# Performance work log

Hardware: AMD Instinct MI355X
Metric: run time of the kernel (lower is better)

Reference implementation:

```python
import jax, jax.numpy as jnp
import numpy as np

N = 50000          # num nodes
E = 800000         # num edges (before self loops)
DIM_IN = 128
HID = 32           # per-head hidden of conv1
HEADS = 8          # heads of conv1
DIM_OUT = 16       # output classes (conv2, 1 head, concat=False)
NEG_SLOPE = 0.2    # GATConv default leaky_relu slope


def gat_conv(x, W, a_src, a_dst, bias, src, dst, heads, out_ch, concat):
    """PyG GATConv (self-loops already appended to src/dst).
    x: [N, F_in], W: [F_in, heads*out_ch], a_src/a_dst: [heads, out_ch], bias matches output.
    """
    n = x.shape[0]
    h = (x @ W).reshape(n, heads, out_ch)                    # [N, H, C]
    al_src = jnp.einsum('nhc,hc->nh', h, a_src)              # [N, H]
    al_dst = jnp.einsum('nhc,hc->nh', h, a_dst)              # [N, H]
    e = jax.nn.leaky_relu(al_src[src] + al_dst[dst], NEG_SLOPE)   # [E', H]
    # segment softmax over edges grouped by target node (dst)
    emax = jax.ops.segment_max(e, dst, num_segments=n)       # [N, H]
    ee = jnp.exp(e - emax[dst])                              # [E', H]
    denom = jax.ops.segment_sum(ee, dst, num_segments=n)     # [N, H]
    alpha = ee / (denom[dst] + 1e-16)                        # [E', H]
    msg = h[src] * alpha[:, :, None]                         # [E', H, C]
    out = jax.ops.segment_sum(msg, dst, num_segments=n)      # [N, H, C]
    out = out.reshape(n, heads * out_ch) if concat else out.mean(axis=1)
    return out + bias


def setup_inputs() -> dict:
    key = jax.random.key(0)
    ks = jax.random.split(key, 12)
    x = jax.random.normal(ks[0], (N, DIM_IN), dtype=jnp.float32)
    edge_index = jax.random.randint(ks[1], (2, E), 0, N, dtype=jnp.int64)
    s = 0.1
    W1 = jax.random.normal(ks[2], (DIM_IN, HEADS * HID), dtype=jnp.float32) * s
    a1_src = jax.random.normal(ks[3], (HEADS, HID), dtype=jnp.float32) * s
    a1_dst = jax.random.normal(ks[4], (HEADS, HID), dtype=jnp.float32) * s
    b1 = jnp.zeros((HEADS * HID,), dtype=jnp.float32)
    W2 = jax.random.normal(ks[5], (HEADS * HID, DIM_OUT), dtype=jnp.float32) * s
    a2_src = jax.random.normal(ks[6], (1, DIM_OUT), dtype=jnp.float32) * s
    a2_dst = jax.random.normal(ks[7], (1, DIM_OUT), dtype=jnp.float32) * s
    b2 = jnp.zeros((DIM_OUT,), dtype=jnp.float32)
    return {"x": x, "edge_index": edge_index, "W1": W1, "a1_src": a1_src,
            "a1_dst": a1_dst, "b1": b1, "W2": W2, "a2_src": a2_src,
            "a2_dst": a2_dst, "b2": b2}


def reference(x, edge_index, W1, a1_src, a1_dst, b1, W2, a2_src, a2_dst, b2):
    # add self loops (GATConv default add_self_loops=True)
    loops = jnp.arange(N, dtype=edge_index.dtype)
    src = jnp.concatenate([edge_index[0], loops])
    dst = jnp.concatenate([edge_index[1], loops])
    # dropout layers are identity in eval mode
    h = gat_conv(x, W1, a1_src, a1_dst, b1, src, dst, HEADS, HID, concat=True)
    h = jax.nn.elu(h)
    out = gat_conv(h, W2, a2_src, a2_dst, b2, src, dst, 1, DIM_OUT, concat=False)
    return jax.nn.log_softmax(out, axis=1)
```

## Files before the change

kernel.cpp:

```cpp
#include <hip/hip_runtime.h>
#include <hip/hip_bf16.h>

#define NN 50000
#define EE 800000
#define EP (EE + NN)
#define DIN 128
#define HID 32
#define HEADS 8
#define C1 (HEADS * HID)
#define DOUT 16
#define NW1 3125
#define SH 8
#define NB 196
#define CAP 8192
#define EPT 8
#define BBLK (256 * EPT)
#define GB ((NW1 * 64 + 255) / 256)
#define BB ((EP + BBLK - 1) / BBLK)

typedef __attribute__((ext_vector_type(8))) short short8;
typedef __attribute__((ext_vector_type(4))) float float4v;
typedef __attribute__((ext_vector_type(2))) float float2v;

__device__ inline unsigned short f2bf(float f) {
    __hip_bfloat16 b = __float2bfloat16(f);
    return *reinterpret_cast<unsigned short*>(&b);
}
__device__ inline float bflo(unsigned u) {
    union { unsigned int i; float f; } x;
    x.i = u << 16;
    return x.f;
}
__device__ inline float bfhi(unsigned u) {
    union { unsigned int i; float f; } x;
    x.i = u & 0xffff0000u;
    return x.f;
}
__device__ inline float bf2f(unsigned short u) {
    union { unsigned int i; float f; } x;
    x.i = ((unsigned int)u) << 16;
    return x.f;
}

__global__ void k_prepfw(const float* __restrict__ W1, const float* __restrict__ a1s,
                         const float* __restrict__ a1d, const float* __restrict__ W2,
                         unsigned short* __restrict__ w1frag,
                         unsigned short* __restrict__ w2frag,
                         int* __restrict__ cntb) {
    int i = blockIdx.x * 256 + threadIdx.x;
    if (blockIdx.x == 0 && threadIdx.x < NB) cntb[threadIdx.x] = 0;
    if (i < 17 * 2048) {
        int j = i & 7, lane = (i >> 3) & 63, s = (i >> 9) & 3, c = i >> 11;
        int q = lane >> 4, m = lane & 15;
        int k = s * 32 + q * 8 + j;
        float val;
        if (c < 16) {
            val = W1[k * C1 + c * 16 + m];
        } else {
            int h = m & 7;
            const float* av = (m < 8) ? a1s : a1d;
            float acc = 0.f;
            #pragma unroll
            for (int j2 = 0; j2 < 32; j2++)
                acc += W1[k * C1 + h * 32 + j2] * av[h * 32 + j2];
            val = acc;
        }
        w1frag[i] = f2bf(val);
    } else if (i < 17 * 2048 + 8 * 512) {
        int j2 = i - 17 * 2048;
        int jj = j2 & 7, lane = (j2 >> 3) & 63, s = j2 >> 9;
        int q = lane >> 4, m = lane & 15;
        w2frag[j2] = f2bf(W2[(s * 32 + q * 8 + jj) * DOUT + m]);
    }
}

__global__ __launch_bounds__(256) void k_g1bkt(const float* __restrict__ x,
                                               const unsigned short* __restrict__ w1frag,
                                               unsigned char* __restrict__ h1f8,
                                               float* __restrict__ al1sd,
                                               unsigned short* __restrict__ al1s8,
                                               const int* __restrict__ ei,
                                               int* __restrict__ cntb,
                                               unsigned* __restrict__ ebuf) {
    __shared__ int hist[4][NB];
    __shared__ int base[4][NB];
    int bid = blockIdx.x;
    if (bid < GB) {
        int wid = (bid * 256 + threadIdx.x) >> 6;
        int lane = threadIdx.x & 63;
        if (wid >= NW1) return;
        int nb = wid * 16;
        int m = lane & 15, quad = lane >> 4;
        const float* xrow = x + (nb + m) * DIN;

        float4 xf[8];
        #pragma unroll
        for (int s = 0; s < 4; s++) {
            xf[2 * s]     = *(const float4*)(xrow + s * 32 + quad * 8);
            xf[2 * s + 1] = *(const float4*)(xrow + s * 32 + quad * 8 + 4);
        }
        short8 bfr[4];
        #pragma unroll
        for (int s = 0; s < 4; s++) {
            unsigned short* bp = (unsigned short*)&bfr[s];
            float4 f0 = xf[2 * s], f1 = xf[2 * s + 1];
            bp[0] = f2bf(f0.x); bp[1] = f2bf(f0.y); bp[2] = f2bf(f0.z); bp[3] = f2bf(f0.w);
            bp[4] = f2bf(f1.x); bp[5] = f2bf(f1.y); bp[6] = f2bf(f1.z); bp[7] = f2bf(f1.w);
        }

        float4v acc[17];
        #pragma unroll
        for (int c = 0; c < 17; c++) acc[c] = (float4v){0.f, 0.f, 0.f, 0.f};

        #pragma unroll
        for (int s = 0; s < 4; s++) {
            const unsigned short* fp = w1frag + (s * 64 + lane) * 8;
            #pragma unroll
            for (int c = 0; c < 17; c++) {
                short8 afrag = *(const short8*)(fp + c * 2048);
                acc[c] = __builtin_amdgcn_mfma_f32_16x16x32_bf16(afrag, bfr[s], acc[c], 0, 0, 0);
            }
        }

        int node = nb + m;
        #pragma unroll
        for (int c = 0; c < 16; c++) {
            unsigned pk = 0;
            pk = __builtin_amdgcn_cvt_pk_fp8_f32(acc[c][0], acc[c][1], pk, false);
            pk = __builtin_amdgcn_cvt_pk_fp8_f32(acc[c][2], acc[c][3], pk, true);
            *(unsigned*)(h1f8 + node * C1 + c * 16 + quad * 4) = pk;
        }
        *(float4*)(al1sd + node * 16 + quad * 4) =
            make_float4(acc[16][0], acc[16][1], acc[16][2], acc[16][3]);
        if (quad < 2) {
            uint2 pk;
            pk.x = (unsigned)f2bf(acc[16][0]) | ((unsigned)f2bf(acc[16][1]) << 16);
            pk.y = (unsigned)f2bf(acc[16][2]) | ((unsigned)f2bf(acc[16][3]) << 16);
            *(uint2*)(al1s8 + node * 8 + quad * 4) = pk;
        }
    } else {
        int t = threadIdx.x;
        int wave = t >> 6;
        for (int i = t; i < 4 * NB; i += 256) ((int*)hist)[i] = 0;
        __syncthreads();
        int e0 = (bid - GB) * BBLK;
        int s[EPT], d[EPT], r[EPT];
        #pragma unroll
        for (int j = 0; j < EPT; j++) {
            int e = e0 + j * 256 + t;
            int ss = 0, dd = -1;
            if (e < EE) { ss = ei[e]; dd = ei[EE + e]; }
            else if (e < EP) { ss = e - EE; dd = ss; }
            s[j] = ss; d[j] = dd;
            if (dd >= 0) r[j] = atomicAdd(&hist[wave][dd >> SH], 1);
        }
        __syncthreads();
        if (t < NB) {
            int h0 = hist[0][t], h1 = hist[1][t], h2 = hist[2][t], h3 = hist[3][t];
            int tot = h0 + h1 + h2 + h3;
            int bb = tot ? atomicAdd(&cntb[t], tot) : 0;
            base[0][t] = bb;
            base[1][t] = bb + h0;
            base[2][t] = bb + h0 + h1;
            base[3][t] = bb + h0 + h1 + h2;
        }
        __syncthreads();
        #pragma unroll
        for (int j = 0; j < EPT; j++) {
            if (d[j] >= 0) {
                int b = d[j] >> SH;
                ebuf[b * CAP + base[wave][b] + r[j]] =
                    ((unsigned)s[j] << SH) | (unsigned)(d[j] & 255);
            }
        }
    }
}

__global__ __launch_bounds__(1024) void k_csr(const int* __restrict__ cntb,
                                              const unsigned* __restrict__ ebuf,
                                              int* __restrict__ row_ptr,
                                              int* __restrict__ esrc) {
    __shared__ int sdeg[256];
    __shared__ int wtot[4];
    __shared__ int bpart[4];
    int b = blockIdx.x;
    int t = threadIdx.x;
    int lane = t & 63, wave = t >> 6;
    int nodes0 = b << SH;
    if (t < 256) sdeg[t] = 0;
    if (t < 256) {
        int v = (t < b) ? cntb[t] : 0;
        #pragma unroll
        for (int off = 1; off < 64; off <<= 1) v += __shfl_xor(v, off, 64);
        if (lane == 0) bpart[wave] = v;
    }
    __syncthreads();
    int baseS = bpart[0] + bpart[1] + bpart[2] + bpart[3];
    int cnt = cntb[b];
    const unsigned* eb = ebuf + b * CAP;
    for (int i = t; i < cnt; i += 1024)
        atomicAdd(&sdeg[eb[i] & 255], 1);
    __syncthreads();
    int v = (t < 256) ? sdeg[t] : 0;
    int inc = v;
    #pragma unroll
    for (int off = 1; off < 64; off <<= 1) {
        int u = __shfl_up(inc, off, 64);
        if (lane >= off) inc += u;
    }
    if (t < 256 && lane == 63) wtot[wave] = inc;
    __syncthreads();
    if (wave == 0 && lane < 4) {
        int w = wtot[lane];
        int iw = w;
        #pragma unroll
        for (int off = 1; off < 4; off <<= 1) {
            int u = __shfl_up(iw, off, 64);
            if (lane >= off) iw += u;
        }
        wtot[lane] = iw - w;
    }
    __syncthreads();
    int excl = inc - v + ((t < 256) ? wtot[wave] : 0);
    __syncthreads();
    if (t < 256) {
        sdeg[t] = excl;
        int node = nodes0 + t;
        if (node < NN) row_ptr[node] = baseS + excl;
    }
    __syncthreads();
    for (int i = t; i < cnt; i += 1024) {
        unsigned e = eb[i];
        int pos = atomicAdd(&sdeg[e & 255], 1);
        esrc[baseS + pos] = (int)(e >> SH);
    }
    if (b == 0 && t == 0) row_ptr[NN] = EP;
}

__global__ __launch_bounds__(256) void k_agg1(const int* __restrict__ row_ptr,
                                              const int* __restrict__ esrc,
                                              const unsigned short* __restrict__ al1s8,
                                              const float* __restrict__ al1sd,
                                              const unsigned char* __restrict__ h1f8,
                                              const float* __restrict__ b1,
                                              unsigned short* __restrict__ helu_b) {
    int L = threadIdx.x & 63;
    int d = __builtin_amdgcn_readfirstlane((int)((blockIdx.x * 256 + threadIdx.x) >> 6));
    int start = row_ptr[d], end = row_ptr[d + 1];
    const int Lofs = L * 4;
    const int hprod = L & 7;
    const int egrp  = L >> 3;
    float ald_p = al1sd[d * 16 + 8 + hprod];
    float denom = 0.f;
    float4 acc = make_float4(0.f, 0.f, 0.f, 0.f);

    for (int base = start; base < end; base += 32) {
        int cnt = min(32, end - base);
        int sval = d;
        if (L < cnt) sval = esrc[base + L];
        float asv0, asv1, asv2, asv3;
        {
            int sp0 = __shfl(sval, 0 * 8 + egrp, 64);
            int sp1 = __shfl(sval, 1 * 8 + egrp, 64);
            int sp2 = __shfl(sval, 2 * 8 + egrp, 64);
            int sp3 = __shfl(sval, 3 * 8 + egrp, 64);
            asv0 = bf2f(al1s8[sp0 * 8 + hprod]);
            asv1 = bf2f(al1s8[sp1 * 8 + hprod]);
            asv2 = bf2f(al1s8[sp2 * 8 + hprod]);
            asv3 = bf2f(al1s8[sp3 * 8 + hprod]);
        }
        #define AGG1_GROUP(K, ASV)                                              \
        if (cnt > (K) * 8) {                                                    \
            float e = (ASV) + ald_p;                                            \
            e = e > 0.f ? e : 0.2f * e;                                         \
            float w = ((K) * 8 + egrp < cnt) ? __expf(e) : 0.f;                 \
            unsigned v[8];                                                      \
            float xw[8];                                                        \
            _Pragma("unroll")                                                   \
            for (int j = 0; j < 8; j++) {                                       \
                int sj = __builtin_amdgcn_readlane(sval, (K) * 8 + j);          \
                v[j] = *(const unsigned*)(h1f8 + sj * C1 + Lofs);               \
                xw[j] = __shfl(w, j * 8 + egrp, 64);                            \
            }                                                                   \
            _Pragma("unroll")                                                   \
            for (int j = 0; j < 8; j++) {                                       \
                float2v a = __builtin_amdgcn_cvt_pk_f32_fp8(v[j], false);       \
                float2v b = __builtin_amdgcn_cvt_pk_f32_fp8(v[j], true);        \
                float xj = xw[j];                                               \
                denom += xj;                                                    \
                acc.x += xj * a.x; acc.y += xj * a.y;                           \
                acc.z += xj * b.x; acc.w += xj * b.y;                           \
            }                                                                   \
        }
        AGG1_GROUP(0, asv0)
        AGG1_GROUP(1, asv1)
        AGG1_GROUP(2, asv2)
        AGG1_GROUP(3, asv3)
        #undef AGG1_GROUP
    }
    float inv = 1.0f / (denom + 1e-16f);
    float4 bv = *(const float4*)(b1 + Lofs);
    float o0 = acc.x * inv + bv.x;
    float o1 = acc.y * inv + bv.y;
    float o2 = acc.z * inv + bv.z;
    float o3 = acc.w * inv + bv.w;
    o0 = o0 > 0.f ? o0 : __expf(o0) - 1.0f;
    o1 = o1 > 0.f ? o1 : __expf(o1) - 1.0f;
    o2 = o2 > 0.f ? o2 : __expf(o2) - 1.0f;
    o3 = o3 > 0.f ? o3 : __expf(o3) - 1.0f;
    uint2 pk;
    pk.x = (unsigned)f2bf(o0) | ((unsigned)f2bf(o1) << 16);
    pk.y = (unsigned)f2bf(o2) | ((unsigned)f2bf(o3) << 16);
    *(uint2*)(helu_b + d * C1 + Lofs) = pk;
}

__global__ __launch_bounds__(256) void k_gemm2(const unsigned short* __restrict__ helu_b,
                                               const unsigned short* __restrict__ w2frag,
                                               const float* __restrict__ a2s,
                                               const float* __restrict__ a2d,
                                               unsigned short* __restrict__ h2b,
                                               float* __restrict__ al2s,
                                               float* __restrict__ al2d) {
    int wid = (blockIdx.x * 256 + threadIdx.x) >> 6;
    int lane = threadIdx.x & 63;
    int nb = wid * 16;
    if (nb >= NN) return;
    int m = lane & 15, quad = lane >> 4;

    const unsigned short* wp2 = w2frag + lane * 8;
    float4v acc = {0.f, 0.f, 0.f, 0.f};
    const unsigned short* arow = helu_b + (nb + m) * C1 + quad * 8;
    #pragma unroll
    for (int s = 0; s < 8; s++) {
        short8 afrag = *(const short8*)(arow + s * 32);
        short8 bfrag = *(const short8*)(wp2 + s * 512);
        acc = __builtin_amdgcn_mfma_f32_16x16x32_bf16(afrag, bfrag, acc, 0, 0, 0);
    }

    float as_c = a2s[m], ad_c = a2d[m];
    #pragma unroll
    for (int r = 0; r < 4; r++) {
        int node = nb + quad * 4 + r;
        float val = acc[r];
        h2b[node * DOUT + m] = f2bf(val);
        float ps = val * as_c;
        float pd = val * ad_c;
        ps += __shfl_xor(ps, 1, 64); ps += __shfl_xor(ps, 2, 64);
        ps += __shfl_xor(ps, 4, 64); ps += __shfl_xor(ps, 8, 64);
        pd += __shfl_xor(pd, 1, 64); pd += __shfl_xor(pd, 2, 64);
        pd += __shfl_xor(pd, 4, 64); pd += __shfl_xor(pd, 8, 64);
        if (m == 0) {
            al2s[node] = ps;
            al2d[node] = pd;
        }
    }
}

__global__ __launch_bounds__(256) void k_agg2(const int* __restrict__ row_ptr,
                                              const int* __restrict__ esrc,
                                              const unsigned short* __restrict__ h2b,
                                              const float* __restrict__ al2s,
                                              const float* __restrict__ al2d,
                                              const float* __restrict__ b2,
                                              float* __restrict__ out) {
    int L = threadIdx.x & 63;
    int n = __builtin_amdgcn_readfirstlane((int)((blockIdx.x * 256 + threadIdx.x) >> 6));
    int p = L & 7, g = L >> 3;
    int start = row_ptr[n], end = row_ptr[n + 1];
    float ald = al2d[n];
    float acc0 = 0.f, acc1 = 0.f, denom = 0.f;

    for (int base = start; base < end; base += 64) {
        int cnt = min(64, end - base);
        int sval = n; float w = 0.f;
        if (L < cnt) {
            sval = esrc[base + L];
            float e = al2s[sval] + ald;
            e = e > 0.f ? e : 0.2f * e;
            w = __expf(e);
        }
        unsigned v0, v1, v2, v3, v4, v5, v6, v7;
        float w0, w1, w2, w3, w4, w5, w6, w7;
        #define AGG2_LOAD(K, V, W)                                             \
        if (cnt > (K) * 8) {                                                   \
            int ss = __shfl(sval, (K) * 8 + g, 64);                            \
            W = __shfl(w, (K) * 8 + g, 64);                                    \
            V = *(const unsigned*)(h2b + ss * DOUT + p * 2);                   \
        }
        AGG2_LOAD(0, v0, w0) AGG2_LOAD(1, v1, w1)
        AGG2_LOAD(2, v2, w2) AGG2_LOAD(3, v3, w3)
        AGG2_LOAD(4, v4, w4) AGG2_LOAD(5, v5, w5)
        AGG2_LOAD(6, v6, w6) AGG2_LOAD(7, v7, w7)
        #undef AGG2_LOAD
        #define AGG2_ACC(K, V, W)                                              \
        if (cnt > (K) * 8) {                                                   \
            acc0 += W * bflo(V); acc1 += W * bfhi(V); denom += W;              \
        }
        AGG2_ACC(0, v0, w0) AGG2_ACC(1, v1, w1)
        AGG2_ACC(2, v2, w2) AGG2_ACC(3, v3, w3)
        AGG2_ACC(4, v4, w4) AGG2_ACC(5, v5, w5)
        AGG2_ACC(6, v6, w6) AGG2_ACC(7, v7, w7)
        #undef AGG2_ACC
    }
    acc0 += __shfl_xor(acc0, 8, 64);  acc0 += __shfl_xor(acc0, 16, 64);  acc0 += __shfl_xor(acc0, 32, 64);
    acc1 += __shfl_xor(acc1, 8, 64);  acc1 += __shfl_xor(acc1, 16, 64);  acc1 += __shfl_xor(acc1, 32, 64);
    denom += __shfl_xor(denom, 8, 64); denom += __shfl_xor(denom, 16, 64); denom += __shfl_xor(denom, 32, 64);
    float inv = 1.0f / (denom + 1e-16f);
    float2 bv = *(const float2*)(b2 + p * 2);
    float val0 = acc0 * inv + bv.x;
    float val1 = acc1 * inv + bv.y;
    float m = fmaxf(val0, val1);
    #pragma unroll
    for (int mm = 1; mm < 8; mm <<= 1) m = fmaxf(m, __shfl_xor(m, mm, 64));
    float se = __expf(val0 - m) + __expf(val1 - m);
    #pragma unroll
    for (int mm = 1; mm < 8; mm <<= 1) se += __shfl_xor(se, mm, 64);
    float lse = m + __logf(se);
    if (L < 8) {
        float2 o = make_float2(val0 - lse, val1 - lse);
        *(float2*)(out + n * DOUT + p * 2) = o;
    }
}

extern "C" void kernel_launch(void* const* d_in, const int* in_sizes, int n_in,
                              void* d_out, int out_size, void* d_ws, size_t ws_size,
                              hipStream_t stream) {
    const float* x   = (const float*)d_in[0];
    const int*   ei  = (const int*)d_in[1];
    const float* W1  = (const float*)d_in[2];
    const float* a1s = (const float*)d_in[3];
    const float* a1d = (const float*)d_in[4];
    const float* b1  = (const float*)d_in[5];
    const float* W2  = (const float*)d_in[6];
    const float* a2s = (const float*)d_in[7];
    const float* a2d = (const float*)d_in[8];
    const float* b2  = (const float*)d_in[9];
    float* outp = (float*)d_out;

    unsigned char* h1f8    = (unsigned char*)d_ws;
    unsigned short* helu_b = (unsigned short*)(h1f8 + NN * C1);
    unsigned short* h2b    = helu_b + NN * C1;
    unsigned short* w2frag = h2b + NN * DOUT;
    unsigned short* w1frag = w2frag + 8 * 512;
    unsigned short* al1s8  = w1frag + 17 * 2048;
    float* al1sd = (float*)(al1s8 + NN * 8);
    float* al2sb = al1sd + NN * 16;
    float* al2db = al2sb + NN;
    int* row_ptr = (int*)(al2db + NN);
    int* esrc    = row_ptr + NN + 1;
    int* cntb    = esrc + EP;
    unsigned* ebuf = (unsigned*)helu_b;

    k_prepfw<<<(17 * 2048 + 8 * 512 + 255) / 256, 256, 0, stream>>>(W1, a1s, a1d, W2, w1frag, w2frag, cntb);
    k_g1bkt<<<GB + BB, 256, 0, stream>>>(x, w1frag, h1f8, al1sd, al1s8, ei, cntb, ebuf);
    k_csr<<<NB, 1024, 0, stream>>>(cntb, ebuf, row_ptr, esrc);
    k_agg1<<<12500, 256, 0, stream>>>(row_ptr, esrc, al1s8, al1sd, h1f8, b1, helu_b);
    k_gemm2<<<(NW1 * 64 + 255) / 256, 256, 0, stream>>>(helu_b, w2frag, a2s, a2d, h2b, al2sb, al2db);
    k_agg2<<<(NN * 64 + 255) / 256, 256, 0, stream>>>(row_ptr, esrc, h2b, al2sb, al2db, b2, outp);
}
```

Measured before the change: 189.8 us.

## Fuse second-layer projection and attention logits into layer-1 aggregation epilogue

The separate MFMA GEMM2 kernel is removed. Each wave in k_agg1 now multiplies its node's 256-channel ELU output by a transposed fp32 W2 held in workspace, then reduces across lanes with a transpose-style shuffle scheme to produce the 16 outputs and the layer-2 attention logits. This avoids writing and re-reading the 50000x256 bf16 hidden tensor and saves one kernel launch. In exchange each wave issues 16 float4 weight loads and many cross-lane shuffles, and the matmul now runs on fp32 FMA instead of matrix cores.

New measurement: 206.1 us. +8.6%, slower.

```diff
diff --git a/kernel.cpp b/kernel.cpp
--- a/kernel.cpp
+++ b/kernel.cpp
@@ -45,7 +45,7 @@
 __global__ void k_prepfw(const float* __restrict__ W1, const float* __restrict__ a1s,
                          const float* __restrict__ a1d, const float* __restrict__ W2,
                          unsigned short* __restrict__ w1frag,
-                         unsigned short* __restrict__ w2frag,
+                         float* __restrict__ W2t,
                          int* __restrict__ cntb) {
     int i = blockIdx.x * 256 + threadIdx.x;
     if (blockIdx.x == 0 && threadIdx.x < NB) cntb[threadIdx.x] = 0;
@@ -66,11 +66,10 @@
             val = acc;
         }
         w1frag[i] = f2bf(val);
-    } else if (i < 17 * 2048 + 8 * 512) {
+    } else if (i < 17 * 2048 + DOUT * C1) {
         int j2 = i - 17 * 2048;
-        int jj = j2 & 7, lane = (j2 >> 3) & 63, s = j2 >> 9;
-        int q = lane >> 4, m = lane & 15;
-        w2frag[j2] = f2bf(W2[(s * 32 + q * 8 + jj) * DOUT + m]);
+        int col = j2 >> 8, ch = j2 & 255;
+        W2t[col * C1 + ch] = W2[ch * DOUT + col];
     }
 }
 
@@ -243,7 +242,12 @@
                                               const float* __restrict__ al1sd,
                                               const unsigned char* __restrict__ h1f8,
                                               const float* __restrict__ b1,
-                                              unsigned short* __restrict__ helu_b) {
+                                              const float* __restrict__ W2t,
+                                              const float* __restrict__ a2s,
+                                              const float* __restrict__ a2d,
+                                              unsigned short* __restrict__ h2b,
+                                              float* __restrict__ al2s,
+                                              float* __restrict__ al2d) {
     int L = threadIdx.x & 63;
     int d = __builtin_amdgcn_readfirstlane((int)((blockIdx.x * 256 + threadIdx.x) >> 6));
     int start = row_ptr[d], end = row_ptr[d + 1];
@@ -308,52 +312,58 @@
     o1 = o1 > 0.f ? o1 : __expf(o1) - 1.0f;
     o2 = o2 > 0.f ? o2 : __expf(o2) - 1.0f;
     o3 = o3 > 0.f ? o3 : __expf(o3) - 1.0f;
-    uint2 pk;
-    pk.x = (unsigned)f2bf(o0) | ((unsigned)f2bf(o1) << 16);
-    pk.y = (unsigned)f2bf(o2) | ((unsigned)f2bf(o3) << 16);
-    *(uint2*)(helu_b + d * C1 + Lofs) = pk;
-}
-
-__global__ __launch_bounds__(256) void k_gemm2(const unsigned short* __restrict__ helu_b,
-                                               const unsigned short* __restrict__ w2frag,
-                                               const float* __restrict__ a2s,
-                                               const float* __restrict__ a2d,
-                                               unsigned short* __restrict__ h2b,
-                                               float* __restrict__ al2s,
-                                               float* __restrict__ al2d) {
-    int wid = (blockIdx.x * 256 + threadIdx.x) >> 6;
-    int lane = threadIdx.x & 63;
-    int nb = wid * 16;
-    if (nb >= NN) return;
-    int m = lane & 15, quad = lane >> 4;
-
-    const unsigned short* wp2 = w2frag + lane * 8;
-    float4v acc = {0.f, 0.f, 0.f, 0.f};
-    const unsigned short* arow = helu_b + (nb + m) * C1 + quad * 8;
-    #pragma unroll
-    for (int s = 0; s < 8; s++) {
-        short8 afrag = *(const short8*)(arow + s * 32);
-        short8 bfrag = *(const short8*)(wp2 + s * 512);
-        acc = __builtin_amdgcn_mfma_f32_16x16x32_bf16(afrag, bfrag, acc, 0, 0, 0);
-    }
-
-    float as_c = a2s[m], ad_c = a2d[m];
-    #pragma unroll
-    for (int r = 0; r < 4; r++) {
-        int node = nb + quad * 4 + r;
-        float val = acc[r];
-        h2b[node * DOUT + m] = f2bf(val);
-        float ps = val * as_c;
-        float pd = val * ad_c;
-        ps += __shfl_xor(ps, 1, 64); ps += __shfl_xor(ps, 2, 64);
-        ps += __shfl_xor(ps, 4, 64); ps += __shfl_xor(ps, 8, 64);
-        pd += __shfl_xor(pd, 1, 64); pd += __shfl_xor(pd, 2, 64);
-        pd += __shfl_xor(pd, 4, 64); pd += __shfl_xor(pd, 8, 64);
-        if (m == 0) {
-            al2s[node] = ps;
-            al2d[node] = pd;
-        }
-    }
+
+    float c[16];
+    {
+        const float* wt = W2t + 4 * L;
+        #pragma unroll
+        for (int k = 0; k < 16; k++) {
+            float4 wr = *(const float4*)(wt + k * C1);
+            c[k] = o0 * wr.x + o1 * wr.y + o2 * wr.z + o3 * wr.w;
+        }
+    }
+    #pragma unroll
+    for (int k = 0; k < 16; k++) {
+        c[k] += __shfl_xor(c[k], 1, 64);
+        c[k] += __shfl_xor(c[k], 2, 64);
+    }
+    int b2 = (L >> 2) & 1, b3 = (L >> 3) & 1, b4 = (L >> 4) & 1, b5 = (L >> 5) & 1;
+    #pragma unroll
+    for (int k = 0; k < 8; k++) {
+        float give = b2 ? c[k] : c[k + 8];
+        float keep = b2 ? c[k + 8] : c[k];
+        c[k] = keep + __shfl_xor(give, 4, 64);
+    }
+    #pragma unroll
+    for (int k = 0; k < 4; k++) {
+        float give = b3 ? c[k] : c[k + 4];
+        float keep = b3 ? c[k + 4] : c[k];
+        c[k] = keep + __shfl_xor(give, 8, 64);
+    }
+    #pragma unroll
+    for (int k = 0; k < 2; k++) {
+        float give = b4 ? c[k] : c[k + 2];
+        float keep = b4 ? c[k + 2] : c[k];
+        c[k] = keep + __shfl_xor(give, 16, 64);
+    }
+    {
+        float give = b5 ? c[0] : c[1];
+        float keep = b5 ? c[1] : c[0];
+        c[0] = keep + __shfl_xor(give, 32, 64);
+    }
+    int col = (b2 << 3) | (b3 << 2) | (b4 << 1) | b5;
+    float cf = c[0];
+    float ps = cf * a2s[col];
+    float pd = cf * a2d[col];
+    ps += __shfl_xor(ps, 4, 64);  ps += __shfl_xor(ps, 8, 64);
+    ps += __shfl_xor(ps, 16, 64); ps += __shfl_xor(ps, 32, 64);
+    pd += __shfl_xor(pd, 4, 64);  pd += __shfl_xor(pd, 8, 64);
+    pd += __shfl_xor(pd, 16, 64); pd += __shfl_xor(pd, 32, 64);
+    if (L == 0) {
+        al2s[d] = ps;
+        al2d[d] = pd;
+    }
+    if ((L & 3) == 0) h2b[d * DOUT + col] = f2bf(cf);
 }
 
 __global__ __launch_bounds__(256) void k_agg2(const int* __restrict__ row_ptr,
@@ -438,23 +448,21 @@
     float* outp = (float*)d_out;
 
     unsigned char* h1f8    = (unsigned char*)d_ws;
-    unsigned short* helu_b = (unsigned short*)(h1f8 + NN * C1);
-    unsigned short* h2b    = helu_b + NN * C1;
-    unsigned short* w2frag = h2b + NN * DOUT;
-    unsigned short* w1frag = w2frag + 8 * 512;
+    unsigned* ebuf = (unsigned*)(h1f8 + NN * C1);
+    unsigned short* h2b    = (unsigned short*)(ebuf + NB * CAP);
+    unsigned short* w1frag = h2b + NN * DOUT;
     unsigned short* al1s8  = w1frag + 17 * 2048;
-    float* al1sd = (float*)(al1s8 + NN * 8);
+    float* W2t   = (float*)(al1s8 + NN * 8);
+    float* al1sd = W2t + DOUT * C1;
     float* al2sb = al1sd + NN * 16;
     float* al2db = al2sb + NN;
     int* row_ptr = (int*)(al2db + NN);
     int* esrc    = row_ptr + NN + 1;
     int* cntb    = esrc + EP;
-    unsigned* ebuf = (unsigned*)helu_b;
-
-    k_prepfw<<<(17 * 2048 + 8 * 512 + 255) / 256, 256, 0, stream>>>(W1, a1s, a1d, W2, w1frag, w2frag, cntb);
+
+    k_prepfw<<<(17 * 2048 + DOUT * C1 + 255) / 256, 256, 0, stream>>>(W1, a1s, a1d, W2, w1frag, W2t, cntb);
     k_g1bkt<<<GB + BB, 256, 0, stream>>>(x, w1frag, h1f8, al1sd, al1s8, ei, cntb, ebuf);
     k_csr<<<NB, 1024, 0, stream>>>(cntb, ebuf, row_ptr, esrc);
-    k_agg1<<<12500, 256, 0, stream>>>(row_ptr, esrc, al1s8, al1sd, h1f8, b1, helu_b);
-    k_gemm2<<<(NW1 * 64 + 255) / 256, 256, 0, stream>>>(helu_b, w2frag, a2s, a2d, h2b, al2sb, al2db);
+    k_agg1<<<12500, 256, 0, stream>>>(row_ptr, esrc, al1s8, al1sd, h1f8, b1, W2t, a2s, a2d, h2b, al2sb, al2db);
     k_agg2<<<(NN * 64 + 255) / 256, 256, 0, stream>>>(row_ptr, esrc, h2b, al2sb, al2db, b2, outp);
 }
```
